# Performance work log

Hardware: AMD Instinct MI355X
Metric: run time of the kernel (lower is better)

Reference implementation:

```python
import jax, jax.numpy as jnp
import numpy as np

B, S, D, H = 4, 2048, 1024, 16
DH = D // H


def setup_inputs() -> dict:
    key = jax.random.key(0)
    ks = jax.random.split(key, 11)
    s = 1.0 / np.sqrt(D)
    return {
        "q": jax.random.normal(ks[0], (B, S, D), jnp.float32),
        "k": jax.random.normal(ks[1], (B, S, D), jnp.float32),
        "v": jax.random.normal(ks[2], (B, S, D), jnp.float32),
        "Wq": jax.random.normal(ks[3], (D, D), jnp.float32) * s,
        "bq": jnp.zeros((D,), jnp.float32),
        "Wk": jax.random.normal(ks[4], (D, D), jnp.float32) * s,
        "bk": jnp.zeros((D,), jnp.float32),
        "Wv": jax.random.normal(ks[5], (D, D), jnp.float32) * s,
        "bv": jnp.zeros((D,), jnp.float32),
        "Wo": jax.random.normal(ks[6], (D, D), jnp.float32) * s,
        "bo": jnp.zeros((D,), jnp.float32),
    }


def _split_heads(x):
    # (B, S, D) -> (B, H, S, DH)
    b, s, _ = x.shape
    return x.reshape(b, s, H, DH).transpose(0, 2, 1, 3)


def reference(q, k, v, Wq, bq, Wk, bk, Wv, bv, Wo, bo):
    # torch Linear: x @ W.T + b
    qh = _split_heads(q @ Wq.T + bq)
    kh = _split_heads(k @ Wk.T + bk)
    vh = _split_heads(v @ Wv.T + bv)
    scale = 1.0 / jnp.sqrt(jnp.asarray(DH, qh.dtype))
    scores = jnp.einsum("bhqd,bhkd->bhqk", qh, kh) * scale  # (B,H,S,S)
    probs = jax.nn.softmax(scores, axis=-1)
    ctx = jnp.einsum("bhqk,bhkd->bhqd", probs, vh)  # (B,H,S,DH)
    x = ctx.transpose(0, 2, 1, 3).reshape(q.shape[0], -1, D)
    return x @ Wo.T + bo
```

## Files before the change

### kernel.cpp

```cpp
#include <hip/hip_runtime.h>

typedef __bf16 bf16x8 __attribute__((ext_vector_type(8)));
typedef __bf16 bf16x4 __attribute__((ext_vector_type(4)));
typedef _Float16 f16x4v __attribute__((ext_vector_type(4)));
typedef float f32x4 __attribute__((ext_vector_type(4)));
typedef float f32x16 __attribute__((ext_vector_type(16)));
typedef unsigned short u16;
typedef unsigned int u32;

constexpr int Bc = 4, Sc = 2048, Dc = 1024, Hc = 16, DHc = 64;
constexpr int Mrows = Bc * Sc;
constexpr size_t MK = (size_t)Mrows * Dc;
constexpr size_t WK = (size_t)Dc * Dc;

__device__ __forceinline__ u16 f2bf(float f) {
  u32 u = __float_as_uint(f);
  u = (u + 0x7fffu + ((u >> 16) & 1u)) >> 16;
  return (u16)u;
}

#define LDSP(p) ((__attribute__((address_space(3))) void*)(p))
#define GLBP(p) ((const __attribute__((address_space(1))) void*)(p))

__global__ __launch_bounds__(256) void cvt3_kernel(const float* __restrict__ a,
                                                   const float* __restrict__ b,
                                                   const float* __restrict__ c,
                                                   ushort4* __restrict__ out, int n4) {
  const float4* in = (const float4*)(blockIdx.y == 0 ? a : blockIdx.y == 1 ? b : c);
  ushort4* o = out + (size_t)blockIdx.y * n4;
  int stride = gridDim.x * blockDim.x;
  for (int i = blockIdx.x * blockDim.x + threadIdx.x; i < n4; i += stride) {
    float4 v = in[i];
    ushort4 r;
    r.x = f2bf(v.x); r.y = f2bf(v.y); r.z = f2bf(v.z); r.w = f2bf(v.w);
    o[i] = r;
  }
}

__global__ __launch_bounds__(256) void cvt4_kernel(const float* __restrict__ a,
                                                   const float* __restrict__ b,
                                                   const float* __restrict__ c,
                                                   const float* __restrict__ d,
                                                   ushort4* __restrict__ out, int n4) {
  const float4* in = (const float4*)(blockIdx.y == 0 ? a : blockIdx.y == 1 ? b
                                     : blockIdx.y == 2 ? c : d);
  ushort4* o = out + (size_t)blockIdx.y * n4;
  int stride = gridDim.x * blockDim.x;
  for (int i = blockIdx.x * blockDim.x + threadIdx.x; i < n4; i += stride) {
    float4 v = in[i];
    ushort4 r;
    r.x = f2bf(v.x); r.y = f2bf(v.y); r.z = f2bf(v.z); r.w = f2bf(v.w);
    o[i] = r;
  }
}

template <int FUSED3>
__global__ __launch_bounds__(512, 2) void gemm8(const u16* __restrict__ A0,
                                                const u16* __restrict__ Bt0,
                                                const float* __restrict__ b0,
                                                const float* __restrict__ b1,
                                                const float* __restrict__ b2,
                                                void* __restrict__ out0) {
  constexpr int K = 1024, NT = 16;
  __shared__ u16 lds[3 * 24576];

  const int y = FUSED3 ? (int)blockIdx.y : 3;
  const u16* A = A0 + (FUSED3 ? (size_t)blockIdx.y * MK : 0);
  const u16* Bt = Bt0 + (FUSED3 ? (size_t)blockIdx.y * WK : 0);
  const float* bias = FUSED3 ? (y == 0 ? b0 : y == 1 ? b1 : b2) : b0;

  const int wg = (blockIdx.x & 7) * 32 + (blockIdx.x >> 3);
  const int tm = wg >> 3, tn = wg & 7;
  const int row0 = tm << 8, col0 = tn << 7;

  const int t_ = threadIdx.x, w = t_ >> 6, l = t_ & 63;
  const int wm = w >> 1, wn = w & 1;
  const int col = l & 31, hh = l >> 5;

  f32x16 acc[2][2] = {};

  auto stA = [&](int tile, int i) {
    u16* buf = &lds[(tile % 3) * 24576];
    const int c = (w * 4 + i) * 64 + l;
    const int r = c >> 3, gl = c & 7;
    __builtin_amdgcn_global_load_lds(
        GLBP(A + (size_t)(row0 + r) * K + (tile << 6) + ((gl ^ (r & 7)) << 3)),
        LDSP(buf + (w * 4 + i) * 512), 16, 0, 0);
  };
  auto stB = [&](int tile, int i) {
    u16* buf = &lds[(tile % 3) * 24576] + 16384;
    const int c = (w * 2 + i) * 64 + l;
    const int r = c >> 3, gl = c & 7;
    __builtin_amdgcn_global_load_lds(
        GLBP(Bt + (size_t)(col0 + r) * K + (tile << 6) + ((gl ^ (r & 7)) << 3)),
        LDSP(buf + (w * 2 + i) * 512), 16, 0, 0);
  };

#pragma unroll
  for (int i = 0; i < 4; ++i) stA(0, i);
#pragma unroll
  for (int i = 0; i < 2; ++i) stB(0, i);
#pragma unroll
  for (int i = 0; i < 4; ++i) stA(1, i);
#pragma unroll
  for (int i = 0; i < 2; ++i) stB(1, i);
  asm volatile("s_waitcnt vmcnt(6)" ::: "memory");
  __builtin_amdgcn_s_barrier();

  const int ar0 = wm * 64 + col, ar1 = ar0 + 32;
  const int br0 = wn * 64 + col, br1 = br0 + 32;

#pragma unroll 1
  for (int t = 0; t < NT; ++t) {
    const u16* abuf = &lds[(t % 3) * 24576];
    const u16* bbuf = abuf + 16384;
#pragma unroll
    for (int ks = 0; ks < 4; ++ks) {
      bf16x8 a0 = *(const bf16x8*)&abuf[ar0 * 64 + ((((ks << 1) + hh) ^ (ar0 & 7)) << 3)];
      bf16x8 a1 = *(const bf16x8*)&abuf[ar1 * 64 + ((((ks << 1) + hh) ^ (ar1 & 7)) << 3)];
      bf16x8 bq0 = *(const bf16x8*)&bbuf[br0 * 64 + ((((ks << 1) + hh) ^ (br0 & 7)) << 3)];
      bf16x8 bq1 = *(const bf16x8*)&bbuf[br1 * 64 + ((((ks << 1) + hh) ^ (br1 & 7)) << 3)];
      if (t + 2 < NT) {
        if (ks == 0) { stA(t + 2, 0); stA(t + 2, 1); }
        else if (ks == 1) { stA(t + 2, 2); stA(t + 2, 3); }
        else if (ks == 2) { stB(t + 2, 0); stB(t + 2, 1); }
      }
      __builtin_amdgcn_sched_barrier(0);
      __builtin_amdgcn_s_barrier();
      __builtin_amdgcn_sched_barrier(0);
      __builtin_amdgcn_s_setprio(1);
      acc[0][0] = __builtin_amdgcn_mfma_f32_32x32x16_bf16(a0, bq0, acc[0][0], 0, 0, 0);
      acc[0][1] = __builtin_amdgcn_mfma_f32_32x32x16_bf16(a0, bq1, acc[0][1], 0, 0, 0);
      acc[1][0] = __builtin_amdgcn_mfma_f32_32x32x16_bf16(a1, bq0, acc[1][0], 0, 0, 0);
      acc[1][1] = __builtin_amdgcn_mfma_f32_32x32x16_bf16(a1, bq1, acc[1][1], 0, 0, 0);
      __builtin_amdgcn_s_setprio(0);
      __builtin_amdgcn_sched_barrier(0);
      if (ks == 3) {
        if (t + 2 < NT)      asm volatile("s_waitcnt vmcnt(6)" ::: "memory");
        else if (t + 1 < NT) asm volatile("s_waitcnt vmcnt(0)" ::: "memory");
      }
      __builtin_amdgcn_s_barrier();
    }
  }

#pragma unroll
  for (int mi = 0; mi < 2; ++mi)
#pragma unroll
    for (int ni = 0; ni < 2; ++ni) {
      const int n = col0 + wn * 64 + ni * 32 + col;
      const float bv = bias[n];
      const int mbase = row0 + wm * 64 + mi * 32 + 4 * hh;
      if (y == 3) {
        float* O = (float*)out0;
#pragma unroll
        for (int r = 0; r < 16; ++r) {
          const int m = mbase + (r & 3) + 8 * (r >> 2);
          O[(size_t)m * Dc + n] = acc[mi][ni][r] + bv;
        }
      } else if (y == 2) {
        u16* Vt = (u16*)out0 + 2 * MK;
        const int h = n >> 6, dh = n & 63;
#pragma unroll
        for (int qg = 0; qg < 4; ++qg) {
          const int s0 = mbase + 8 * qg;
          const int b = s0 >> 11, s = s0 & (Sc - 1);
          f16x4v pk;
#pragma unroll
          for (int r4 = 0; r4 < 4; ++r4) pk[r4] = (_Float16)(acc[mi][ni][qg * 4 + r4] + bv);
          *(f16x4v*)&Vt[((size_t)((b * Hc + h) * DHc + dh)) * Sc + s] = pk;
        }
      } else {
        u16* Oh = (u16*)out0 + (size_t)y * MK;
        const float scl = (y == 0) ? 0.125f * 1.44269504089f : 1.f;
        const int h = n >> 6, dh = n & 63;
#pragma unroll
        for (int r = 0; r < 16; ++r) {
          const int m = mbase + (r & 3) + 8 * (r >> 2);
          const int b = m >> 11, s = m & (Sc - 1);
          Oh[((size_t)((b * Hc + h) * Sc + s)) * DHc + dh] = f2bf((acc[mi][ni][r] + bv) * scl);
        }
      }
    }
}

__global__ __launch_bounds__(256, 2) void attn2_kernel(const u16* __restrict__ Qh,
                                                       const u16* __restrict__ Kh,
                                                       const u16* __restrict__ Vt,
                                                       u16* __restrict__ ctx) {
  __shared__ u16 smem[8192];
  u16* K_lds = smem;
  u16* V_lds = smem + 4096;

  const int wid = (blockIdx.x & 7) * 128 + (blockIdx.x >> 3);
  const int qt = wid & 15, bh = wid >> 4;
  const int t = threadIdx.x, w = t >> 6, l = t & 63;
  const int q = l & 31, h = l >> 5;
  const int q0 = qt * 128 + w * 32;

  bf16x8 qf[4];
  {
    const u16* qp = Qh + ((size_t)bh * Sc + q0 + q) * DHc + h * 8;
#pragma unroll
    for (int kk = 0; kk < 4; ++kk) qf[kk] = *(const bf16x8*)(qp + kk * 16);
  }

  f32x16 oacc[2] = {};
  float m_run = -3.0e38f, l_run = 0.f;

  const int lrow = l >> 3, lg = l & 7;

  for (int kt = 0; kt < Sc; kt += 64) {
    __syncthreads();
#pragma unroll
    for (int c = 0; c < 2; ++c) {
      const int rb = w * 16 + c * 8;
      const int row = rb + lrow;
      const int sg = lg ^ (row & 7);
      __builtin_amdgcn_global_load_lds(GLBP(Kh + ((size_t)bh * Sc + kt + row) * DHc + sg * 8),
                                       LDSP(&K_lds[rb * 64]), 16, 0, 0);
      __builtin_amdgcn_global_load_lds(GLBP(Vt + ((size_t)bh * DHc + row) * Sc + kt + sg * 8),
                                       LDSP(&V_lds[rb * 64]), 16, 0, 0);
    }
    __syncthreads();

    f32x16 sacc[2];
#pragma unroll
    for (int kt32 = 0; kt32 < 2; ++kt32) {
      f32x16 s_ = {};
      const int krow = kt32 * 32 + q;
      __builtin_amdgcn_s_setprio(1);
#pragma unroll
      for (int kk = 0; kk < 4; ++kk) {
        bf16x8 kf = *(const bf16x8*)&K_lds[krow * 64 + ((2 * kk + h) ^ (krow & 7)) * 8];
        s_ = __builtin_amdgcn_mfma_f32_32x32x16_bf16(kf, qf[kk], s_, 0, 0, 0);
      }
      __builtin_amdgcn_s_setprio(0);
      sacc[kt32] = s_;
    }

    float mx;
    {
      float t0 = fmaxf(fmaxf(sacc[0][0], sacc[0][1]), sacc[0][2]);
      float t1 = fmaxf(fmaxf(sacc[0][3], sacc[0][4]), sacc[0][5]);
      float t2 = fmaxf(fmaxf(sacc[0][6], sacc[0][7]), sacc[0][8]);
      float t3 = fmaxf(fmaxf(sacc[0][9], sacc[0][10]), sacc[0][11]);
      float t4 = fmaxf(fmaxf(sacc[0][12], sacc[0][13]), sacc[0][14]);
      float t5 = fmaxf(fmaxf(sacc[0][15], sacc[1][0]), sacc[1][1]);
      float t6 = fmaxf(fmaxf(sacc[1][2], sacc[1][3]), sacc[1][4]);
      float t7 = fmaxf(fmaxf(sacc[1][5], sacc[1][6]), sacc[1][7]);
      float t8 = fmaxf(fmaxf(sacc[1][8], sacc[1][9]), sacc[1][10]);
      float t9 = fmaxf(fmaxf(sacc[1][11], sacc[1][12]), sacc[1][13]);
      float ta = fmaxf(sacc[1][14], sacc[1][15]);
      float u0 = fmaxf(fmaxf(t0, t1), t2);
      float u1 = fmaxf(fmaxf(t3, t4), t5);
      float u2 = fmaxf(fmaxf(t6, t7), t8);
      float u3 = fmaxf(t9, ta);
      mx = fmaxf(fmaxf(u0, u1), fmaxf(u2, u3));
    }
    mx = fmaxf(mx, __shfl_xor(mx, 32));
    if (__any(mx - m_run > 8.f)) {
      const float mnew = fmaxf(m_run, mx);
      const float corr = __builtin_amdgcn_exp2f(m_run - mnew);
      m_run = mnew;
      l_run *= corr;
#pragma unroll
      for (int dt = 0; dt < 2; ++dt)
#pragma unroll
        for (int r = 0; r < 16; ++r) oacc[dt][r] *= corr;
    }
    float sum = 0.f;
    f16x4v pa[2][4];
#pragma unroll
    for (int kt32 = 0; kt32 < 2; ++kt32)
#pragma unroll
      for (int kc = 0; kc < 4; ++kc) {
        float p0 = __builtin_amdgcn_exp2f(sacc[kt32][kc * 4 + 0] - m_run);
        float p1 = __builtin_amdgcn_exp2f(sacc[kt32][kc * 4 + 1] - m_run);
        float p2 = __builtin_amdgcn_exp2f(sacc[kt32][kc * 4 + 2] - m_run);
        float p3 = __builtin_amdgcn_exp2f(sacc[kt32][kc * 4 + 3] - m_run);
        sum += (p0 + p1) + (p2 + p3);
        auto lo = __builtin_amdgcn_cvt_pkrtz(p0, p1);
        auto hi = __builtin_amdgcn_cvt_pkrtz(p2, p3);
        f16x4v pk;
        pk[0] = (_Float16)lo[0]; pk[1] = (_Float16)lo[1];
        pk[2] = (_Float16)hi[0]; pk[3] = (_Float16)hi[1];
        pa[kt32][kc] = pk;
      }
    sum += __shfl_xor(sum, 32);
    l_run += sum;

    __builtin_amdgcn_s_setprio(1);
#pragma unroll
    for (int kt32 = 0; kt32 < 2; ++kt32)
#pragma unroll
      for (int kc = 0; kc < 4; ++kc)
#pragma unroll
        for (int dt = 0; dt < 2; ++dt) {
          const int vrow = dt * 32 + q;
          f16x4v vf = *(const f16x4v*)&V_lds[vrow * 64 + ((kt32 * 4 + kc) ^ (vrow & 7)) * 8 + 4 * h];
          oacc[dt] = __builtin_amdgcn_mfma_f32_32x32x8f16(vf, pa[kt32][kc], oacc[dt], 0, 0, 0);
        }
    __builtin_amdgcn_s_setprio(0);
  }

  __syncthreads();
  const float inv = 1.f / l_run;
  u16* E = smem + w * 2048;
#pragma unroll
  for (int dt = 0; dt < 2; ++dt)
#pragma unroll
    for (int rg = 0; rg < 4; ++rg) {
      bf16x4 pk;
#pragma unroll
      for (int j = 0; j < 4; ++j) pk[j] = (__bf16)(oacc[dt][rg * 4 + j] * inv);
      const int dh0 = dt * 32 + rg * 8 + 4 * h;
      int byte = q * 128 + dh0 * 2;
      byte ^= (q & 7) << 4;
      *(bf16x4*)((char*)E + byte) = pk;
    }
  __syncthreads();
  const int b = bh >> 4, head = bh & 15;
  const size_t crow = ((size_t)(b * Sc + q0 + q)) * Dc + head * 64 + h * 32;
#pragma unroll
  for (int i = 0; i < 4; ++i) {
    const int g = (4 * h + i) ^ (q & 7);
    uint4 tv = *(const uint4*)((char*)E + q * 128 + g * 16);
    *(uint4*)((u16*)ctx + crow + i * 8) = tv;
  }
}

extern "C" void kernel_launch(void* const* d_in, const int* in_sizes, int n_in,
                              void* d_out, int out_size, void* d_ws, size_t ws_size,
                              hipStream_t stream) {
  const float* q  = (const float*)d_in[0];
  const float* k  = (const float*)d_in[1];
  const float* v  = (const float*)d_in[2];
  const float* Wq = (const float*)d_in[3];
  const float* bq = (const float*)d_in[4];
  const float* Wk = (const float*)d_in[5];
  const float* bk = (const float*)d_in[6];
  const float* Wv = (const float*)d_in[7];
  const float* bv = (const float*)d_in[8];
  const float* Wo = (const float*)d_in[9];
  const float* bo = (const float*)d_in[10];
  float* out = (float*)d_out;

  u16* qb  = (u16*)d_ws;
  u16* Wqb = qb + 3 * MK;
  u16* Qh  = Wqb + 4 * WK;
  u16* Kh  = Qh + MK;
  u16* VtB = Kh + MK;
  u16* ctx = VtB + MK;

  cvt3_kernel<<<dim3(2048, 3), 256, 0, stream>>>(q, k, v, (ushort4*)qb, (int)(MK / 4));
  cvt4_kernel<<<dim3(512, 4), 256, 0, stream>>>(Wq, Wk, Wv, Wo, (ushort4*)Wqb, (int)(WK / 4));

  gemm8<1><<<dim3(256, 3), 512, 0, stream>>>(qb, Wqb, bq, bk, bv, (void*)Qh);

  attn2_kernel<<<1024, 256, 0, stream>>>(Qh, Kh, VtB, ctx);

  gemm8<0><<<dim3(256, 1), 512, 0, stream>>>(ctx, Wqb + 3 * WK, bo, bo, bo, (void*)out);
}
```

Measured before the change: 230.8 us.

## Halve barriers in GEMM k-loop and double attention KV tile to 128

The GEMM main loop now handles two k-steps per barrier phase, loading both fragment pairs first and issuing eight MFMAs between barriers. This halves the s_barrier count per tile. The attention kernel loads 128 keys per outer iteration instead of 64, which halves the __syncthreads pairs and doubles LDS use (32KB per block). The risks are higher register pressure and LDS occupancy limits, and the softmax conversion to fp16 now uses a plain cast instead of pkrtz.

```diff
diff --git a/kernel.cpp b/kernel.cpp
--- a/kernel.cpp
+++ b/kernel.cpp
@@ -53,6 +53,8 @@
     o[i] = r;
   }
 }
+
+enum GemmMode { MODE_Q = 0, MODE_K = 1, MODE_V = 2, MODE_OUT = 3 };
 
 template <int FUSED3>
 __global__ __launch_bounds__(512, 2) void gemm8(const u16* __restrict__ A0,
@@ -115,32 +117,37 @@
     const u16* abuf = &lds[(t % 3) * 24576];
     const u16* bbuf = abuf + 16384;
 #pragma unroll
-    for (int ks = 0; ks < 4; ++ks) {
-      bf16x8 a0 = *(const bf16x8*)&abuf[ar0 * 64 + ((((ks << 1) + hh) ^ (ar0 & 7)) << 3)];
-      bf16x8 a1 = *(const bf16x8*)&abuf[ar1 * 64 + ((((ks << 1) + hh) ^ (ar1 & 7)) << 3)];
-      bf16x8 bq0 = *(const bf16x8*)&bbuf[br0 * 64 + ((((ks << 1) + hh) ^ (br0 & 7)) << 3)];
-      bf16x8 bq1 = *(const bf16x8*)&bbuf[br1 * 64 + ((((ks << 1) + hh) ^ (br1 & 7)) << 3)];
+    for (int ph = 0; ph < 2; ++ph) {
+      bf16x8 a0[2], a1[2], q0[2], q1[2];
+#pragma unroll
+      for (int k2 = 0; k2 < 2; ++k2) {
+        const int ks = ph * 2 + k2;
+        a0[k2] = *(const bf16x8*)&abuf[ar0 * 64 + ((((ks << 1) + hh) ^ (ar0 & 7)) << 3)];
+        a1[k2] = *(const bf16x8*)&abuf[ar1 * 64 + ((((ks << 1) + hh) ^ (ar1 & 7)) << 3)];
+        q0[k2] = *(const bf16x8*)&bbuf[br0 * 64 + ((((ks << 1) + hh) ^ (br0 & 7)) << 3)];
+        q1[k2] = *(const bf16x8*)&bbuf[br1 * 64 + ((((ks << 1) + hh) ^ (br1 & 7)) << 3)];
+      }
       if (t + 2 < NT) {
-        if (ks == 0) { stA(t + 2, 0); stA(t + 2, 1); }
-        else if (ks == 1) { stA(t + 2, 2); stA(t + 2, 3); }
-        else if (ks == 2) { stB(t + 2, 0); stB(t + 2, 1); }
+        if (ph == 0) { stA(t + 2, 0); stA(t + 2, 1); stA(t + 2, 2); }
+        else         { stA(t + 2, 3); stB(t + 2, 0); stB(t + 2, 1); }
       }
       __builtin_amdgcn_sched_barrier(0);
       __builtin_amdgcn_s_barrier();
       __builtin_amdgcn_sched_barrier(0);
       __builtin_amdgcn_s_setprio(1);
-      acc[0][0] = __builtin_amdgcn_mfma_f32_32x32x16_bf16(a0, bq0, acc[0][0], 0, 0, 0);
-      acc[0][1] = __builtin_amdgcn_mfma_f32_32x32x16_bf16(a0, bq1, acc[0][1], 0, 0, 0);
-      acc[1][0] = __builtin_amdgcn_mfma_f32_32x32x16_bf16(a1, bq0, acc[1][0], 0, 0, 0);
-      acc[1][1] = __builtin_amdgcn_mfma_f32_32x32x16_bf16(a1, bq1, acc[1][1], 0, 0, 0);
+#pragma unroll
+      for (int k2 = 0; k2 < 2; ++k2) {
+        acc[0][0] = __builtin_amdgcn_mfma_f32_32x32x16_bf16(a0[k2], q0[k2], acc[0][0], 0, 0, 0);
+        acc[0][1] = __builtin_amdgcn_mfma_f32_32x32x16_bf16(a0[k2], q1[k2], acc[0][1], 0, 0, 0);
+        acc[1][0] = __builtin_amdgcn_mfma_f32_32x32x16_bf16(a1[k2], q0[k2], acc[1][0], 0, 0, 0);
+        acc[1][1] = __builtin_amdgcn_mfma_f32_32x32x16_bf16(a1[k2], q1[k2], acc[1][1], 0, 0, 0);
+      }
       __builtin_amdgcn_s_setprio(0);
       __builtin_amdgcn_sched_barrier(0);
-      if (ks == 3) {
-        if (t + 2 < NT)      asm volatile("s_waitcnt vmcnt(6)" ::: "memory");
-        else if (t + 1 < NT) asm volatile("s_waitcnt vmcnt(0)" ::: "memory");
-      }
-      __builtin_amdgcn_s_barrier();
-    }
+    }
+    if (t + 2 < NT)      asm volatile("s_waitcnt vmcnt(6)" ::: "memory");
+    else if (t + 1 < NT) asm volatile("s_waitcnt vmcnt(0)" ::: "memory");
+    __builtin_amdgcn_s_barrier();
   }
 
 #pragma unroll
@@ -183,13 +190,13 @@
     }
 }
 
-__global__ __launch_bounds__(256, 2) void attn2_kernel(const u16* __restrict__ Qh,
+__global__ __launch_bounds__(256, 2) void attn3_kernel(const u16* __restrict__ Qh,
                                                        const u16* __restrict__ Kh,
                                                        const u16* __restrict__ Vt,
                                                        u16* __restrict__ ctx) {
-  __shared__ u16 smem[8192];
+  __shared__ u16 smem[16384];
   u16* K_lds = smem;
-  u16* V_lds = smem + 4096;
+  u16* V_lds = smem + 8192;
 
   const int wid = (blockIdx.x & 7) * 128 + (blockIdx.x >> 3);
   const int qt = wid & 15, bh = wid >> 4;
@@ -207,100 +214,88 @@
   f32x16 oacc[2] = {};
   float m_run = -3.0e38f, l_run = 0.f;
 
-  const int lrow = l >> 3, lg = l & 7;
-
-  for (int kt = 0; kt < Sc; kt += 64) {
+  for (int kt = 0; kt < Sc; kt += 128) {
     __syncthreads();
 #pragma unroll
-    for (int c = 0; c < 2; ++c) {
-      const int rb = w * 16 + c * 8;
-      const int row = rb + lrow;
-      const int sg = lg ^ (row & 7);
+    for (int c = 0; c < 4; ++c) {
+      const int kb = (w * 4 + c) * 8;
+      const int row = kb + (l >> 3);
+      const int sg = (l & 7) ^ (row & 7);
       __builtin_amdgcn_global_load_lds(GLBP(Kh + ((size_t)bh * Sc + kt + row) * DHc + sg * 8),
-                                       LDSP(&K_lds[rb * 64]), 16, 0, 0);
+                                       LDSP(&K_lds[kb * 64]), 16, 0, 0);
+    }
+#pragma unroll
+    for (int c = 0; c < 4; ++c) {
+      const int vb = (w * 4 + c) * 4;
+      const int row = vb + (l >> 4);
+      const int sg = (l & 15) ^ (row & 15);
       __builtin_amdgcn_global_load_lds(GLBP(Vt + ((size_t)bh * DHc + row) * Sc + kt + sg * 8),
-                                       LDSP(&V_lds[rb * 64]), 16, 0, 0);
+                                       LDSP(&V_lds[vb * 128]), 16, 0, 0);
     }
     __syncthreads();
 
-    f32x16 sacc[2];
-#pragma unroll
-    for (int kt32 = 0; kt32 < 2; ++kt32) {
-      f32x16 s_ = {};
-      const int krow = kt32 * 32 + q;
+#pragma unroll
+    for (int h64 = 0; h64 < 2; ++h64) {
+      f32x16 sacc[2];
+#pragma unroll
+      for (int kt32 = 0; kt32 < 2; ++kt32) {
+        f32x16 s_ = {};
+        const int krow = h64 * 64 + kt32 * 32 + q;
+        __builtin_amdgcn_s_setprio(1);
+#pragma unroll
+        for (int kk = 0; kk < 4; ++kk) {
+          bf16x8 kf = *(const bf16x8*)&K_lds[krow * 64 + ((2 * kk + h) ^ (krow & 7)) * 8];
+          s_ = __builtin_amdgcn_mfma_f32_32x32x16_bf16(kf, qf[kk], s_, 0, 0, 0);
+        }
+        __builtin_amdgcn_s_setprio(0);
+        sacc[kt32] = s_;
+      }
+
+      float mx = sacc[0][0];
+#pragma unroll
+      for (int r = 1; r < 16; ++r) mx = fmaxf(mx, sacc[0][r]);
+#pragma unroll
+      for (int r = 0; r < 16; ++r) mx = fmaxf(mx, sacc[1][r]);
+      mx = fmaxf(mx, __shfl_xor(mx, 32));
+      if (__any(mx - m_run > 8.f)) {
+        const float mnew = fmaxf(m_run, mx);
+        const float corr = __builtin_amdgcn_exp2f(m_run - mnew);
+        m_run = mnew;
+        l_run *= corr;
+#pragma unroll
+        for (int dt = 0; dt < 2; ++dt)
+#pragma unroll
+          for (int r = 0; r < 16; ++r) oacc[dt][r] *= corr;
+      }
+      float sum = 0.f;
+      f16x4v pa[2][4];
+#pragma unroll
+      for (int kt32 = 0; kt32 < 2; ++kt32)
+#pragma unroll
+        for (int kc = 0; kc < 4; ++kc)
+#pragma unroll
+          for (int j = 0; j < 4; ++j) {
+            float pv = __builtin_amdgcn_exp2f(sacc[kt32][kc * 4 + j] - m_run);
+            sum += pv;
+            pa[kt32][kc][j] = (_Float16)pv;
+          }
+      sum += __shfl_xor(sum, 32);
+      l_run += sum;
+
       __builtin_amdgcn_s_setprio(1);
 #pragma unroll
-      for (int kk = 0; kk < 4; ++kk) {
-        bf16x8 kf = *(const bf16x8*)&K_lds[krow * 64 + ((2 * kk + h) ^ (krow & 7)) * 8];
-        s_ = __builtin_amdgcn_mfma_f32_32x32x16_bf16(kf, qf[kk], s_, 0, 0, 0);
-      }
+      for (int kt32 = 0; kt32 < 2; ++kt32)
+#pragma unroll
+        for (int kc = 0; kc < 4; ++kc)
+#pragma unroll
+          for (int dt = 0; dt < 2; ++dt) {
+            const int vrow = dt * 32 + q;
+            const int kslot = h64 * 8 + kt32 * 4 + kc;
+            f16x4v vf = *(const f16x4v*)&V_lds[vrow * 128 + ((kslot ^ (vrow & 15)) * 8) + 4 * h];
+            oacc[dt] = __builtin_amdgcn_mfma_f32_32x32x8f16(vf, pa[kt32][kc], oacc[dt], 0, 0, 0);
+          }
       __builtin_amdgcn_s_setprio(0);
-      sacc[kt32] = s_;
-    }
-
-    float mx;
-    {
-      float t0 = fmaxf(fmaxf(sacc[0][0], sacc[0][1]), sacc[0][2]);
-      float t1 = fmaxf(fmaxf(sacc[0][3], sacc[0][4]), sacc[0][5]);
-      float t2 = fmaxf(fmaxf(sacc[0][6], sacc[0][7]), sacc[0][8]);
-      float t3 = fmaxf(fmaxf(sacc[0][9], sacc[0][10]), sacc[0][11]);
-      float t4 = fmaxf(fmaxf(sacc[0][12], sacc[0][13]), sacc[0][14]);
-      float t5 = fmaxf(fmaxf(sacc[0][15], sacc[1][0]), sacc[1][1]);
-      float t6 = fmaxf(fmaxf(sacc[1][2], sacc[1][3]), sacc[1][4]);
-      float t7 = fmaxf(fmaxf(sacc[1][5], sacc[1][6]), sacc[1][7]);
-      float t8 = fmaxf(fmaxf(sacc[1][8], sacc[1][9]), sacc[1][10]);
-      float t9 = fmaxf(fmaxf(sacc[1][11], sacc[1][12]), sacc[1][13]);
-      float ta = fmaxf(sacc[1][14], sacc[1][15]);
-      float u0 = fmaxf(fmaxf(t0, t1), t2);
-      float u1 = fmaxf(fmaxf(t3, t4), t5);
-      float u2 = fmaxf(fmaxf(t6, t7), t8);
-      float u3 = fmaxf(t9, ta);
-      mx = fmaxf(fmaxf(u0, u1), fmaxf(u2, u3));
-    }
-    mx = fmaxf(mx, __shfl_xor(mx, 32));
-    if (__any(mx - m_run > 8.f)) {
-      const float mnew = fmaxf(m_run, mx);
-      const float corr = __builtin_amdgcn_exp2f(m_run - mnew);
-      m_run = mnew;
-      l_run *= corr;
-#pragma unroll
-      for (int dt = 0; dt < 2; ++dt)
-#pragma unroll
-        for (int r = 0; r < 16; ++r) oacc[dt][r] *= corr;
-    }
-    float sum = 0.f;
-    f16x4v pa[2][4];
-#pragma unroll
-    for (int kt32 = 0; kt32 < 2; ++kt32)
-#pragma unroll
-      for (int kc = 0; kc < 4; ++kc) {
-        float p0 = __builtin_amdgcn_exp2f(sacc[kt32][kc * 4 + 0] - m_run);
-        float p1 = __builtin_amdgcn_exp2f(sacc[kt32][kc * 4 + 1] - m_run);
-        float p2 = __builtin_amdgcn_exp2f(sacc[kt32][kc * 4 + 2] - m_run);
-        float p3 = __builtin_amdgcn_exp2f(sacc[kt32][kc * 4 + 3] - m_run);
-        sum += (p0 + p1) + (p2 + p3);
-        auto lo = __builtin_amdgcn_cvt_pkrtz(p0, p1);
-        auto hi = __builtin_amdgcn_cvt_pkrtz(p2, p3);
-        f16x4v pk;
-        pk[0] = (_Float16)lo[0]; pk[1] = (_Float16)lo[1];
-        pk[2] = (_Float16)hi[0]; pk[3] = (_Float16)hi[1];
-        pa[kt32][kc] = pk;
-      }
-    sum += __shfl_xor(sum, 32);
-    l_run += sum;
-
-    __builtin_amdgcn_s_setprio(1);
-#pragma unroll
-    for (int kt32 = 0; kt32 < 2; ++kt32)
-#pragma unroll
-      for (int kc = 0; kc < 4; ++kc)
-#pragma unroll
-        for (int dt = 0; dt < 2; ++dt) {
-          const int vrow = dt * 32 + q;
-          f16x4v vf = *(const f16x4v*)&V_lds[vrow * 64 + ((kt32 * 4 + kc) ^ (vrow & 7)) * 8 + 4 * h];
-          oacc[dt] = __builtin_amdgcn_mfma_f32_32x32x8f16(vf, pa[kt32][kc], oacc[dt], 0, 0, 0);
-        }
-    __builtin_amdgcn_s_setprio(0);
+    }
   }
 
   __syncthreads();
@@ -357,7 +352,7 @@
 
   gemm8<1><<<dim3(256, 3), 512, 0, stream>>>(qb, Wqb, bq, bk, bv, (void*)Qh);
 
-  attn2_kernel<<<1024, 256, 0, stream>>>(Qh, Kh, VtB, ctx);
+  attn3_kernel<<<1024, 256, 0, stream>>>(Qh, Kh, VtB, ctx);
 
   gemm8<0><<<dim3(256, 1), 512, 0, stream>>>(ctx, Wqb + 3 * WK, bo, bo, bo, (void*)out);
 }
```

Result: slower. 236.6 us (+2.5%).
